# Optimization experiments

Measured on AMD Instinct MI355X. Metric: run time of the kernel, lower is better.

The kernel has to match this reference:

```python
import jax, jax.numpy as jnp
import numpy as np

DIM = 256
NUM_HEADS = 8


def setup_inputs() -> dict:
    key = jax.random.key(0)
    ks = jax.random.split(key, 5)
    x = jax.random.normal(ks[0], (32, DIM, 56, 56), dtype=jnp.float32)
    # Conv2d(dim, 2*dim, k=1, groups=2): weight [2*dim, dim//2, 1, 1]
    qk_w = jax.random.normal(ks[1], (2 * DIM, DIM // 2, 1, 1), dtype=jnp.float32) * (DIM // 2) ** -0.5
    qk_b = jax.random.normal(ks[2], (2 * DIM,), dtype=jnp.float32) * 0.02
    # Conv2d(dim, dim, k=3, pad=1, groups=dim): weight [dim, 1, 3, 3]
    pe_w = jax.random.normal(ks[3], (DIM, 1, 3, 3), dtype=jnp.float32) * (1.0 / 3.0)
    pe_b = jax.random.normal(ks[4], (DIM,), dtype=jnp.float32) * 0.02
    return {"x": x, "qk_w": qk_w, "qk_b": qk_b, "pe_w": pe_w, "pe_b": pe_b}


def _conv(x, w, padding, groups):
    return jax.lax.conv_general_dilated(
        x, w, window_strides=(1, 1), padding=padding,
        feature_group_count=groups,
        dimension_numbers=("NCHW", "OIHW", "NCHW"))


def reference(x, qk_w, qk_b, pe_w, pe_b):
    b, c, h, w = x.shape
    H, hd = NUM_HEADS, c // NUM_HEADS
    n = h * w
    s = n ** (-0.5)

    # grouped 1x1 conv -> elu + 1 feature map
    qk = _conv(x, qk_w, "VALID", groups=2) + qk_b[None, :, None, None]
    qk = jax.nn.elu(qk) + 1.0                       # [b, 2c, h, w]
    qk = qk.reshape(b, 2, H, hd, n)
    q, k = qk[:, 0], qk[:, 1]                       # [b, H, hd, n]
    v = x.reshape(b, H, hd, n)                      # [b, H, hd, n]

    # kv = (k*s) @ (v^T * s)  -> [b, H, hd, hd]
    kv = jnp.einsum("bhdn,bhen->bhde", k * s, v * s)
    # numerator: q^T @ kv -> [b, H, n, hd]
    num = jnp.einsum("bhdn,bhde->bhne", q, kv)
    # denominator: q^T @ mean_n(k) -> [b, H, n]
    den = jnp.einsum("bhdn,bhd->bhn", q, k.mean(axis=-1))
    out = num / (den[..., None] + 1e-6)             # [b, H, n, hd]

    out = out.transpose(0, 1, 3, 2).reshape(b, c, h, w)
    pe = _conv(x, pe_w, [(1, 1), (1, 1)], groups=c) + pe_b[None, :, None, None]
    return out + pe
```

## Files before the change

kernel.cpp:

```cpp
#include <hip/hip_runtime.h>
#include <cmath>

#define NCH   256
#define NPIX  3136
#define NB    32
#define SEV   7
#define INV_N (1.0f / 3136.0f)

typedef __attribute__((ext_vector_type(8)))  short bf16x8;
typedef __attribute__((ext_vector_type(4)))  float f32x4;
typedef __attribute__((ext_vector_type(16))) float f32x16;

#define KV7_F  (SEV * NB * 8 * 1024)
#define KM7_F  (SEV * NB * 256)
#define KVF_F  (NB * 8 * 1024)
#define KMF_F  (NB * 256)
#define KM7_OFF (KV7_F)
#define KVF_OFF (KM7_OFF + KM7_F)
#define KMF_OFF (KVF_OFF + KVF_F)
#define WF_OFF  (KMF_OFF + KMF_F)

__device__ __forceinline__ ushort f2bf(float f) {
  unsigned u = __float_as_uint(f);
  u += 0x7FFFu + ((u >> 16) & 1u);
  return (ushort)(u >> 16);
}
__device__ __forceinline__ float bf2f(ushort h) {
  return __uint_as_float(((unsigned)h) << 16);
}

__global__ void wfrag_kernel(const float* __restrict__ qk_w, ushort* __restrict__ Wf) {
  const int tid = blockIdx.x * 512 + threadIdx.x;
  const int lane = tid & 63;
  const int ks = (tid >> 6) & 3;
  const int mt = (tid >> 8) & 15;
  const int hl = (tid >> 12) & 1;
  const int side = (tid >> 13) & 1;
  const int ch = mt * 16 + (lane & 15);
  const int oc = side * 256 + ch;
  ushort v[8];
#pragma unroll
  for (int j = 0; j < 8; ++j) {
    const int k = ks * 32 + (lane >> 4) * 8 + j;
    const float w = qk_w[(size_t)oc * 128 + k];
    const ushort hi = f2bf(w);
    v[j] = (hl == 0) ? hi : f2bf(w - bf2f(hi));
  }
  *(uint4*)(Wf + (size_t)tid * 8) = *(const uint4*)v;
}

__global__ __launch_bounds__(512)
void pe_kernel(const float* __restrict__ x, const float* __restrict__ pe_w,
               const float* __restrict__ pe_b, float* __restrict__ out) {
  const int b = blockIdx.y;
  const int t = threadIdx.x;
  const int w = t >> 6;
  const int l = t & 63;
  const int c = blockIdx.x * 8 + w;

  const bool act = (l < 56);
  const int c4 = act ? (l % 14) : 0;
  const int rq = act ? (l / 14) : 0;
  const int col = c4 * 4;

  const float* xc = x + ((size_t)(b * NCH + c)) * NPIX;
  float* oc = out + ((size_t)(b * NCH + c)) * NPIX;

  float pw[9];
#pragma unroll
  for (int i = 0; i < 9; ++i) pw[i] = pe_w[c * 9 + i];
  const float pb = pe_b[c];
  const float4 Z = {0.f, 0.f, 0.f, 0.f};

  const int aoff = c4 ? (col - 1) : 0;
  const int boff = (c4 < 13) ? (col + 1) : col;

#pragma unroll
  for (int sb = 0; sb < 4; ++sb) {
    const int bi0 = sb * 4 + rq;
    const bool bact = act && (bi0 < 14);
    const int bi = (bi0 < 14) ? bi0 : 13;
    const int r0 = bi * 4;

    float xr[6][6];
#pragma unroll
    for (int j = 0; j < 6; ++j) {
      const int rr = r0 - 1 + j;
      const bool vr = (rr >= 0) && (rr < 56);
      float4 A = Z, B = Z;
      if (vr) {
        A = *(const float4*)(xc + rr * 56 + aoff);
        B = *(const float4*)(xc + rr * 56 + boff);
      }
      xr[j][0] = c4 ? A.x : 0.f;
      xr[j][1] = c4 ? A.y : A.x;
      xr[j][2] = c4 ? A.z : A.y;
      xr[j][3] = c4 ? A.w : A.z;
      xr[j][4] = c4 ? ((c4 < 13) ? B.z : B.w) : A.w;
      xr[j][5] = (c4 < 13) ? B.w : 0.f;
    }

#pragma unroll
    for (int k = 0; k < 4; ++k) {
      float res[4];
#pragma unroll
      for (int i = 0; i < 4; ++i) {
        float s = pb;
#pragma unroll
        for (int dy = 0; dy < 3; ++dy) {
          s += pw[dy * 3 + 0] * xr[k + dy][i] +
               pw[dy * 3 + 1] * xr[k + dy][i + 1] +
               pw[dy * 3 + 2] * xr[k + dy][i + 2];
        }
        res[i] = s;
      }
      if (bact) {
        const float4 r4 = {res[0], res[1], res[2], res[3]};
        *(float4*)(oc + (r0 + k) * 56 + col) = r4;
      }
    }
  }
}

__global__ __launch_bounds__(512, 4)
void kv_kernel(const float* __restrict__ x, const ushort* __restrict__ Wf,
               const float* __restrict__ qk_b, float* __restrict__ kv7,
               float* __restrict__ km7) {
  const int bid = blockIdx.x;
  const int hd = (bid >= 224) ? 1 : 0;
  const int rem = bid - hd * 224;
  const int sev = rem >> 5, b = rem & 31;
  const int t = threadIdx.x;
  const int w = t >> 6, l = t & 63;
  const int q = l >> 4, r15 = l & 15;
  const int e = l & 31, q5 = l >> 5;
  const int h_l = w & 3, ph = w >> 2;
  const int mt = w;

  __shared__ __align__(16) ushort Xb[64][152];
  __shared__ __align__(16) ushort KVs[2 * 128 * 88];
  ushort (*Kst)[88] = (ushort(*)[88])KVs;
  ushort (*Vst)[88] = (ushort(*)[88])(KVs + 128 * 88);

  bf16x8 wf[4][2];
#pragma unroll
  for (int ks = 0; ks < 4; ++ks)
#pragma unroll
    for (int hl = 0; hl < 2; ++hl) {
      const size_t off =
          (size_t)(((((2 + hl) * 16 + (hd * 8 + mt)) * 4 + ks) * 64 + l)) * 8;
      wf[ks][hl] = *(const bf16x8*)(Wf + off);
    }

  float bias[4];
#pragma unroll
  for (int r = 0; r < 4; ++r)
    bias[r] = qk_b[256 + hd * 128 + mt * 16 + q * 4 + r];

  f32x16 kvacc;
#pragma unroll
  for (int i = 0; i < 16; ++i) kvacc[i] = 0.f;
  float kmacc[4] = {0.f, 0.f, 0.f, 0.f};

  const float* xk = x + ((size_t)(b * NCH) + 128) * NPIX + sev * 448;
  const float* xv = x + ((size_t)(b * NCH)) * NPIX + sev * 448;

  for (int st = 0; st < SEV; ++st) {
    const int p0 = st * 64;
    __syncthreads();

#pragma unroll
    for (int rr = 0; rr < 4; ++rr) {
      const int id = t + 512 * rr;
      const int cc = id >> 4;
      const int pf = id & 15;
      const float4 v = *(const float4*)(xk + (size_t)cc * NPIX + p0 + pf * 4);
      const ushort b0 = f2bf(v.x), b1 = f2bf(v.y), b2 = f2bf(v.z), b3 = f2bf(v.w);
      Xb[pf * 4 + 0][cc] = b0;
      Xb[pf * 4 + 1][cc] = b1;
      Xb[pf * 4 + 2][cc] = b2;
      Xb[pf * 4 + 3][cc] = b3;
      if (hd == 1) {
        const uint2 pk = {(uint)b0 | ((uint)b1 << 16), (uint)b2 | ((uint)b3 << 16)};
        *(uint2*)&Vst[cc][pf * 4] = pk;
      }
    }
    if (hd == 0) {
#pragma unroll
      for (int rr = 0; rr < 4; ++rr) {
        const int id = t + 512 * rr;
        const int cc = id >> 4;
        const int pf = id & 15;
        const float4 v = *(const float4*)(xv + (size_t)cc * NPIX + p0 + pf * 4);
        const uint2 pk = {(uint)f2bf(v.x) | ((uint)f2bf(v.y) << 16),
                          (uint)f2bf(v.z) | ((uint)f2bf(v.w) << 16)};
        *(uint2*)&Vst[cc][pf * 4] = pk;
      }
    }
    __syncthreads();

    f32x4 acc[4];
#pragma unroll
    for (int nt = 0; nt < 4; ++nt)
#pragma unroll
      for (int r = 0; r < 4; ++r) acc[nt][r] = 0.f;
#pragma unroll
    for (int ks = 0; ks < 4; ++ks) {
      bf16x8 xbf[4];
#pragma unroll
      for (int nt = 0; nt < 4; ++nt)
        xbf[nt] = *(const bf16x8*)&Xb[nt * 16 + r15][ks * 32 + q * 8];
#pragma unroll
      for (int nt = 0; nt < 4; ++nt) {
        acc[nt] = __builtin_amdgcn_mfma_f32_16x16x32_bf16(wf[ks][0], xbf[nt], acc[nt], 0, 0, 0);
        acc[nt] = __builtin_amdgcn_mfma_f32_16x16x32_bf16(wf[ks][1], xbf[nt], acc[nt], 0, 0, 0);
      }
    }

#pragma unroll
    for (int nt = 0; nt < 4; ++nt) {
#pragma unroll
      for (int r = 0; r < 4; ++r) {
        float v = acc[nt][r] + bias[r];
        v = (v > 0.f) ? (v + 1.f) : __expf(v);
        kmacc[r] += v;
        Kst[mt * 16 + q * 4 + r][nt * 16 + r15] = f2bf(v);
      }
    }
    __syncthreads();

#pragma unroll
    for (int ks2 = 0; ks2 < 2; ++ks2) {
      const int kp = ph * 32 + ks2 * 16 + q5 * 8;
      const bf16x8 ak = *(const bf16x8*)&Kst[h_l * 32 + e][kp];
      const bf16x8 bv = *(const bf16x8*)&Vst[h_l * 32 + e][kp];
      kvacc = __builtin_amdgcn_mfma_f32_32x32x16_bf16(ak, bv, kvacc, 0, 0, 0);
    }
  }

  __syncthreads();
  float* red = (float*)KVs;
#pragma unroll
  for (int reg = 0; reg < 16; ++reg) {
    const int row = (reg & 3) + 8 * (reg >> 2) + 4 * q5;
    red[w * 1024 + row * 32 + e] = kvacc[reg];
  }
  __syncthreads();
#pragma unroll
  for (int i = 0; i < 8; ++i) {
    const int idx = t + 512 * i;
    const int hl2 = idx >> 10;
    const int el = idx & 1023;
    const float s = red[hl2 * 1024 + el] + red[(hl2 + 4) * 1024 + el];
    kv7[(((size_t)sev * NB + b) * 8 + hd * 4 + hl2) * 1024 + el] = s;
  }
#pragma unroll
  for (int r = 0; r < 4; ++r) {
    float s = kmacc[r];
    s += __shfl_xor(s, 1);
    s += __shfl_xor(s, 2);
    s += __shfl_xor(s, 4);
    s += __shfl_xor(s, 8);
    if (r15 == 0)
      km7[((size_t)sev * NB + b) * 256 + hd * 128 + mt * 16 + q * 4 + r] = s;
  }
}

__global__ void red_kernel(const float* __restrict__ kv7, const float* __restrict__ km7,
                           float* __restrict__ kvF, float* __restrict__ kmF) {
  const int b = blockIdx.x;
  const int t = threadIdx.x;
  for (int i = t; i < 8192; i += 256) {
    float s = 0.f;
#pragma unroll
    for (int sv = 0; sv < SEV; ++sv)
      s += kv7[(size_t)(sv * NB + b) * 8192 + i];
    kvF[(size_t)b * 8192 + i] = s * INV_N;
  }
  {
    float s = 0.f;
#pragma unroll
    for (int sv = 0; sv < SEV; ++sv)
      s += km7[(size_t)(sv * NB + b) * 256 + t];
    kmF[b * 256 + t] = s * INV_N;
  }
}

__global__ __launch_bounds__(512, 4)
void out_kernel(const float* __restrict__ x, const ushort* __restrict__ Wf,
                const float* __restrict__ qk_b, const float* __restrict__ kvF,
                const float* __restrict__ kmF, float* __restrict__ out) {
  const int bid = blockIdx.x;
  const int hd = (bid >= 224) ? 1 : 0;
  const int rem = bid - hd * 224;
  const int b = rem & 31, sev = rem >> 5;
  const int t = threadIdx.x;
  const int w = t >> 6, l = t & 63;
  const int q = l >> 4, r15 = l & 15;
  const int mt = w;
  const int h_l = w & 3, eh = w >> 2;

  __shared__ ushort Xb[64][136];
  __shared__ ushort QT[64][136];
  __shared__ float denP[8][64];

  bf16x8 wf[4][2];
#pragma unroll
  for (int ks = 0; ks < 4; ++ks)
#pragma unroll
    for (int hl = 0; hl < 2; ++hl) {
      const size_t off =
          (size_t)((((hl * 16 + (hd * 8 + mt)) * 4 + ks) * 64 + l)) * 8;
      wf[ks][hl] = *(const bf16x8*)(Wf + off);
    }

  float bias[4], kmw[4];
#pragma unroll
  for (int r = 0; r < 4; ++r) {
    const int c = hd * 128 + mt * 16 + q * 4 + r;
    bias[r] = qk_b[c];
    kmw[r] = kmF[b * 256 + c];
  }

  bf16x8 bkv;
  {
    const int hg = hd * 4 + h_l;
#pragma unroll
    for (int j = 0; j < 8; ++j)
      bkv[j] = (short)f2bf(
          kvF[(size_t)b * 8192 + hg * 1024 + (q * 8 + j) * 32 + eh * 16 + r15]);
  }

  const float* xq = x + (size_t)(b * NCH) * NPIX + sev * 448;

  for (int st = 0; st < SEV; ++st) {
    const int pos0 = st * 64;
#pragma unroll
    for (int rr = 0; rr < 4; ++rr) {
      const int id = t + 512 * rr;
      const int ch = id >> 4;
      const int p4 = (id & 15) * 4;
      const float4 v = *(const float4*)(xq + (size_t)ch * NPIX + pos0 + p4);
      Xb[p4 + 0][ch] = f2bf(v.x);
      Xb[p4 + 1][ch] = f2bf(v.y);
      Xb[p4 + 2][ch] = f2bf(v.z);
      Xb[p4 + 3][ch] = f2bf(v.w);
    }
    __syncthreads();

    f32x4 acc[4];
#pragma unroll
    for (int nt = 0; nt < 4; ++nt)
#pragma unroll
      for (int r = 0; r < 4; ++r) acc[nt][r] = 0.f;
#pragma unroll
    for (int ks = 0; ks < 4; ++ks) {
      bf16x8 xbf[4];
#pragma unroll
      for (int nt = 0; nt < 4; ++nt)
        xbf[nt] = *(const bf16x8*)&Xb[nt * 16 + r15][ks * 32 + q * 8];
#pragma unroll
      for (int nt = 0; nt < 4; ++nt) {
        acc[nt] = __builtin_amdgcn_mfma_f32_16x16x32_bf16(wf[ks][0], xbf[nt], acc[nt], 0, 0, 0);
        acc[nt] = __builtin_amdgcn_mfma_f32_16x16x32_bf16(wf[ks][1], xbf[nt], acc[nt], 0, 0, 0);
      }
    }

#pragma unroll
    for (int nt = 0; nt < 4; ++nt) {
      ushort pk[4];
      float dsum = 0.f;
#pragma unroll
      for (int r = 0; r < 4; ++r) {
        float v = acc[nt][r] + bias[r];
        v = (v > 0.f) ? (v + 1.f) : __expf(v);
        pk[r] = f2bf(v);
        dsum += v * kmw[r];
      }
      *(uint2*)&QT[nt * 16 + r15][mt * 16 + q * 4] = *(const uint2*)pk;
      dsum += __shfl_xor(dsum, 16);
      dsum += __shfl_xor(dsum, 32);
      if (q == 0) denP[mt][nt * 16 + r15] = dsum;
    }
    __syncthreads();

#pragma unroll
    for (int pt = 0; pt < 4; ++pt) {
      const bf16x8 aq = *(const bf16x8*)&QT[pt * 16 + r15][h_l * 32 + q * 8];
      f32x4 z;
      z[0] = z[1] = z[2] = z[3] = 0.f;
      const f32x4 n0 = __builtin_amdgcn_mfma_f32_16x16x32_bf16(aq, bkv, z, 0, 0, 0);
      float rdn[4];
#pragma unroll
      for (int r = 0; r < 4; ++r) {
        const int pl = pt * 16 + q * 4 + r;
        rdn[r] = 1.0f / (denP[2 * h_l][pl] + denP[2 * h_l + 1][pl] + 1e-6f);
      }
      const int posg = sev * 448 + pos0 + pt * 16 + q * 4;
      const int c = hd * 128 + h_l * 32 + eh * 16 + r15;
      float* op = out + ((size_t)(b * NCH + c)) * NPIX + posg;
      float4 prev = *(const float4*)op;
      prev.x += n0[0] * rdn[0];
      prev.y += n0[1] * rdn[1];
      prev.z += n0[2] * rdn[2];
      prev.w += n0[3] * rdn[3];
      *(float4*)op = prev;
    }
    __syncthreads();
  }
}

extern "C" void kernel_launch(void* const* d_in, const int* in_sizes, int n_in,
                              void* d_out, int out_size, void* d_ws,
                              size_t ws_size, hipStream_t stream) {
  const float* x    = (const float*)d_in[0];
  const float* qk_w = (const float*)d_in[1];
  const float* qk_b = (const float*)d_in[2];
  const float* pe_w = (const float*)d_in[3];
  const float* pe_b = (const float*)d_in[4];
  float* out = (float*)d_out;

  float* wsf = (float*)d_ws;
  float* kv7 = wsf;
  float* km7 = wsf + KM7_OFF;
  float* kvF = wsf + KVF_OFF;
  float* kmF = wsf + KMF_OFF;
  ushort* Wf = (ushort*)(wsf + WF_OFF);

  dim3 gp(32, NB);
  pe_kernel<<<gp, 512, 0, stream>>>(x, pe_w, pe_b, out);
  wfrag_kernel<<<32, 512, 0, stream>>>(qk_w, Wf);
  kv_kernel<<<448, 512, 0, stream>>>(x, Wf, qk_b, kv7, km7);
  red_kernel<<<NB, 256, 0, stream>>>(kv7, km7, kvF, kmF);
  out_kernel<<<448, 512, 0, stream>>>(x, Wf, qk_b, kvF, kmF, out);
}
```

Before: 143.5 us.

## Fuse depthwise positional conv into the kv reduction kernel

```diff
diff --git a/kernel.cpp b/kernel.cpp
--- a/kernel.cpp
+++ b/kernel.cpp
@@ -49,83 +49,11 @@
   *(uint4*)(Wf + (size_t)tid * 8) = *(const uint4*)v;
 }
 
-__global__ __launch_bounds__(512)
-void pe_kernel(const float* __restrict__ x, const float* __restrict__ pe_w,
-               const float* __restrict__ pe_b, float* __restrict__ out) {
-  const int b = blockIdx.y;
-  const int t = threadIdx.x;
-  const int w = t >> 6;
-  const int l = t & 63;
-  const int c = blockIdx.x * 8 + w;
-
-  const bool act = (l < 56);
-  const int c4 = act ? (l % 14) : 0;
-  const int rq = act ? (l / 14) : 0;
-  const int col = c4 * 4;
-
-  const float* xc = x + ((size_t)(b * NCH + c)) * NPIX;
-  float* oc = out + ((size_t)(b * NCH + c)) * NPIX;
-
-  float pw[9];
-#pragma unroll
-  for (int i = 0; i < 9; ++i) pw[i] = pe_w[c * 9 + i];
-  const float pb = pe_b[c];
-  const float4 Z = {0.f, 0.f, 0.f, 0.f};
-
-  const int aoff = c4 ? (col - 1) : 0;
-  const int boff = (c4 < 13) ? (col + 1) : col;
-
-#pragma unroll
-  for (int sb = 0; sb < 4; ++sb) {
-    const int bi0 = sb * 4 + rq;
-    const bool bact = act && (bi0 < 14);
-    const int bi = (bi0 < 14) ? bi0 : 13;
-    const int r0 = bi * 4;
-
-    float xr[6][6];
-#pragma unroll
-    for (int j = 0; j < 6; ++j) {
-      const int rr = r0 - 1 + j;
-      const bool vr = (rr >= 0) && (rr < 56);
-      float4 A = Z, B = Z;
-      if (vr) {
-        A = *(const float4*)(xc + rr * 56 + aoff);
-        B = *(const float4*)(xc + rr * 56 + boff);
-      }
-      xr[j][0] = c4 ? A.x : 0.f;
-      xr[j][1] = c4 ? A.y : A.x;
-      xr[j][2] = c4 ? A.z : A.y;
-      xr[j][3] = c4 ? A.w : A.z;
-      xr[j][4] = c4 ? ((c4 < 13) ? B.z : B.w) : A.w;
-      xr[j][5] = (c4 < 13) ? B.w : 0.f;
-    }
-
-#pragma unroll
-    for (int k = 0; k < 4; ++k) {
-      float res[4];
-#pragma unroll
-      for (int i = 0; i < 4; ++i) {
-        float s = pb;
-#pragma unroll
-        for (int dy = 0; dy < 3; ++dy) {
-          s += pw[dy * 3 + 0] * xr[k + dy][i] +
-               pw[dy * 3 + 1] * xr[k + dy][i + 1] +
-               pw[dy * 3 + 2] * xr[k + dy][i + 2];
-        }
-        res[i] = s;
-      }
-      if (bact) {
-        const float4 r4 = {res[0], res[1], res[2], res[3]};
-        *(float4*)(oc + (r0 + k) * 56 + col) = r4;
-      }
-    }
-  }
-}
-
 __global__ __launch_bounds__(512, 4)
-void kv_kernel(const float* __restrict__ x, const ushort* __restrict__ Wf,
-               const float* __restrict__ qk_b, float* __restrict__ kv7,
-               float* __restrict__ km7) {
+void kvpe_kernel(const float* __restrict__ x, const ushort* __restrict__ Wf,
+                 const float* __restrict__ qk_b, const float* __restrict__ pe_w,
+                 const float* __restrict__ pe_b, float* __restrict__ kv7,
+                 float* __restrict__ km7, float* __restrict__ out) {
   const int bid = blockIdx.x;
   const int hd = (bid >= 224) ? 1 : 0;
   const int rem = bid - hd * 224;
@@ -264,6 +192,63 @@
     if (r15 == 0)
       km7[((size_t)sev * NB + b) * 256 + hd * 128 + mt * 16 + q * 4 + r] = s;
   }
+
+  const bool pact = (l < 56);
+  const int c4 = pact ? (l % 14) : 0;
+  const int rq = pact ? (l / 14) : 0;
+  const int col = c4 * 4;
+  const int aoff = c4 ? (col - 1) : 0;
+  const int boff = (c4 < 13) ? (col + 1) : col;
+  const int row0 = sev * 8 + rq * 2;
+  const float4 Z = {0.f, 0.f, 0.f, 0.f};
+
+  for (int ci = 0; ci < 16; ++ci) {
+    const int c = hd * 128 + w * 16 + ci;
+    const float* xc = x + ((size_t)(b * NCH + c)) * NPIX;
+    float* oc = out + ((size_t)(b * NCH + c)) * NPIX;
+    float pw[9];
+#pragma unroll
+    for (int i = 0; i < 9; ++i) pw[i] = pe_w[c * 9 + i];
+    const float pb = pe_b[c];
+
+    float xr[4][6];
+#pragma unroll
+    for (int j = 0; j < 4; ++j) {
+      const int rr = row0 - 1 + j;
+      const bool vr = (rr >= 0) && (rr < 56);
+      float4 A = Z, B = Z;
+      if (vr) {
+        A = *(const float4*)(xc + rr * 56 + aoff);
+        B = *(const float4*)(xc + rr * 56 + boff);
+      }
+      xr[j][0] = c4 ? A.x : 0.f;
+      xr[j][1] = c4 ? A.y : A.x;
+      xr[j][2] = c4 ? A.z : A.y;
+      xr[j][3] = c4 ? A.w : A.z;
+      xr[j][4] = c4 ? ((c4 < 13) ? B.z : B.w) : A.w;
+      xr[j][5] = (c4 < 13) ? B.w : 0.f;
+    }
+
+#pragma unroll
+    for (int k = 0; k < 2; ++k) {
+      float res[4];
+#pragma unroll
+      for (int i = 0; i < 4; ++i) {
+        float s = pb;
+#pragma unroll
+        for (int dy = 0; dy < 3; ++dy) {
+          s += pw[dy * 3 + 0] * xr[k + dy][i] +
+               pw[dy * 3 + 1] * xr[k + dy][i + 1] +
+               pw[dy * 3 + 2] * xr[k + dy][i + 2];
+        }
+        res[i] = s;
+      }
+      if (pact) {
+        const float4 r4 = {res[0], res[1], res[2], res[3]};
+        *(float4*)(oc + (row0 + k) * 56 + col) = r4;
+      }
+    }
+  }
 }
 
 __global__ void red_kernel(const float* __restrict__ kv7, const float* __restrict__ km7,
@@ -427,10 +412,8 @@
   float* kmF = wsf + KMF_OFF;
   ushort* Wf = (ushort*)(wsf + WF_OFF);
 
-  dim3 gp(32, NB);
-  pe_kernel<<<gp, 512, 0, stream>>>(x, pe_w, pe_b, out);
   wfrag_kernel<<<32, 512, 0, stream>>>(qk_w, Wf);
-  kv_kernel<<<448, 512, 0, stream>>>(x, Wf, qk_b, kv7, km7);
+  kvpe_kernel<<<448, 512, 0, stream>>>(x, Wf, qk_b, pe_w, pe_b, kv7, km7, out);
   red_kernel<<<NB, 256, 0, stream>>>(kv7, km7, kvF, kmF);
   out_kernel<<<448, 512, 0, stream>>>(x, Wf, qk_b, kvF, kmF, out);
 }
```

Result: no change. 144.8 us (+0.9%).

## Remap depthwise conv to block-per-4-channels with flat coalesced pixel indexing

Applied to the files above, without the earlier changes.

```diff
diff --git a/kernel.cpp b/kernel.cpp
--- a/kernel.cpp
+++ b/kernel.cpp
@@ -52,71 +52,64 @@
 __global__ __launch_bounds__(512)
 void pe_kernel(const float* __restrict__ x, const float* __restrict__ pe_w,
                const float* __restrict__ pe_b, float* __restrict__ out) {
-  const int b = blockIdx.y;
+  const int gb = blockIdx.x;
+  const int b = gb >> 6;
+  const int c0 = (gb & 63) * 4;
   const int t = threadIdx.x;
-  const int w = t >> 6;
-  const int l = t & 63;
-  const int c = blockIdx.x * 8 + w;
-
-  const bool act = (l < 56);
-  const int c4 = act ? (l % 14) : 0;
-  const int rq = act ? (l / 14) : 0;
-  const int col = c4 * 4;
-
-  const float* xc = x + ((size_t)(b * NCH + c)) * NPIX;
-  float* oc = out + ((size_t)(b * NCH + c)) * NPIX;
-
-  float pw[9];
-#pragma unroll
-  for (int i = 0; i < 9; ++i) pw[i] = pe_w[c * 9 + i];
-  const float pb = pe_b[c];
   const float4 Z = {0.f, 0.f, 0.f, 0.f};
 
-  const int aoff = c4 ? (col - 1) : 0;
-  const int boff = (c4 < 13) ? (col + 1) : col;
-
-#pragma unroll
-  for (int sb = 0; sb < 4; ++sb) {
-    const int bi0 = sb * 4 + rq;
-    const bool bact = act && (bi0 < 14);
-    const int bi = (bi0 < 14) ? bi0 : 13;
-    const int r0 = bi * 4;
-
-    float xr[6][6];
-#pragma unroll
-    for (int j = 0; j < 6; ++j) {
-      const int rr = r0 - 1 + j;
-      const bool vr = (rr >= 0) && (rr < 56);
-      float4 A = Z, B = Z;
-      if (vr) {
-        A = *(const float4*)(xc + rr * 56 + aoff);
-        B = *(const float4*)(xc + rr * 56 + boff);
-      }
-      xr[j][0] = c4 ? A.x : 0.f;
-      xr[j][1] = c4 ? A.y : A.x;
-      xr[j][2] = c4 ? A.z : A.y;
-      xr[j][3] = c4 ? A.w : A.z;
-      xr[j][4] = c4 ? ((c4 < 13) ? B.z : B.w) : A.w;
-      xr[j][5] = (c4 < 13) ? B.w : 0.f;
-    }
-
-#pragma unroll
-    for (int k = 0; k < 4; ++k) {
-      float res[4];
+  for (int ci = 0; ci < 4; ++ci) {
+    const int c = c0 + ci;
+    const float* xc = x + ((size_t)(b * NCH + c)) * NPIX;
+    float* oc = out + ((size_t)(b * NCH + c)) * NPIX;
+    float pw[9];
+#pragma unroll
+    for (int i = 0; i < 9; ++i) pw[i] = pe_w[c * 9 + i];
+    const float pb = pe_b[c];
+
+#pragma unroll
+    for (int it = 0; it < 2; ++it) {
+      const int qi = t + it * 512;
+      const bool qact = (qi < 784);
+      const int qs = qact ? qi : 783;
+      const int p = qs * 4;
+      const int c4 = (p % 56) >> 2;
+      const int aoff = c4 ? -1 : 0;
+      const int boff = (c4 < 13) ? 1 : 0;
+
+      float xr[3][6];
+#pragma unroll
+      for (int j = 0; j < 3; ++j) {
+        const int pr = p + (j - 1) * 56;
+        const bool vr = (pr >= 0) && (pr < NPIX);
+        float4 A = Z, B = Z;
+        if (vr) {
+          A = *(const float4*)(xc + pr + aoff);
+          B = *(const float4*)(xc + pr + boff);
+        }
+        xr[j][0] = c4 ? A.x : 0.f;
+        xr[j][1] = c4 ? A.y : A.x;
+        xr[j][2] = c4 ? A.z : A.y;
+        xr[j][3] = c4 ? A.w : A.z;
+        xr[j][4] = c4 ? ((c4 < 13) ? B.z : B.w) : A.w;
+        xr[j][5] = (c4 < 13) ? B.w : 0.f;
+      }
+
+      float r_[4];
 #pragma unroll
       for (int i = 0; i < 4; ++i) {
         float s = pb;
 #pragma unroll
         for (int dy = 0; dy < 3; ++dy) {
-          s += pw[dy * 3 + 0] * xr[k + dy][i] +
-               pw[dy * 3 + 1] * xr[k + dy][i + 1] +
-               pw[dy * 3 + 2] * xr[k + dy][i + 2];
+          s += pw[dy * 3 + 0] * xr[dy][i] +
+               pw[dy * 3 + 1] * xr[dy][i + 1] +
+               pw[dy * 3 + 2] * xr[dy][i + 2];
         }
-        res[i] = s;
-      }
-      if (bact) {
-        const float4 r4 = {res[0], res[1], res[2], res[3]};
-        *(float4*)(oc + (r0 + k) * 56 + col) = r4;
+        r_[i] = s;
+      }
+      if (qact) {
+        const float4 r4 = {r_[0], r_[1], r_[2], r_[3]};
+        *(float4*)(oc + p) = r4;
       }
     }
   }
@@ -427,8 +420,7 @@
   float* kmF = wsf + KMF_OFF;
   ushort* Wf = (ushort*)(wsf + WF_OFF);
 
-  dim3 gp(32, NB);
-  pe_kernel<<<gp, 512, 0, stream>>>(x, pe_w, pe_b, out);
+  pe_kernel<<<2048, 512, 0, stream>>>(x, pe_w, pe_b, out);
   wfrag_kernel<<<32, 512, 0, stream>>>(qk_w, Wf);
   kv_kernel<<<448, 512, 0, stream>>>(x, Wf, qk_b, kv7, km7);
   red_kernel<<<NB, 256, 0, stream>>>(kv7, km7, kvF, kmF);
```

After: 144.0 us. No clear change (+0.3%).
